# Performance work log

Measured on AMD Instinct MI355X. Metric: run time of the kernel, lower is better.

The kernel has to match this reference:

```python
import jax, jax.numpy as jnp
import numpy as np
import math

B, T, D, H = 2, 2048, 1024, 16
DK = D // H


def _alibi_bias(n_heads, seq_len):
    # canonical ALiBi: slope_h = 2^(-8*(h+1)/n_heads), bias[h,i,j] = -slope_h * (i - j) for j<=i
    slopes = jnp.asarray([2.0 ** (-8.0 * (h + 1) / n_heads) for h in range(n_heads)], dtype=jnp.float32)
    pos = jnp.arange(seq_len, dtype=jnp.float32)
    dist = pos[None, :] - pos[:, None]              # [T, T], (j - i)
    return slopes[:, None, None] * dist[None, :, :]  # [H, T, T] (masked out above diagonal anyway)


def setup_inputs() -> dict:
    key = jax.random.key(0)
    ks = jax.random.split(key, 8)
    s = 1.0 / math.sqrt(D)
    return {
        "query": jax.random.normal(ks[0], (B, T, D), dtype=jnp.float32),
        "key": jax.random.normal(ks[1], (B, T, D), dtype=jnp.float32),
        "value": jax.random.normal(ks[2], (B, T, D), dtype=jnp.float32),
        "alibi_bias": _alibi_bias(H, T),
        "Wq": jax.random.normal(ks[3], (D, D), dtype=jnp.float32) * s,
        "Wk": jax.random.normal(ks[4], (D, D), dtype=jnp.float32) * s,
        "Wv": jax.random.normal(ks[5], (D, D), dtype=jnp.float32) * s,
        "Wo": jax.random.normal(ks[6], (D, D), dtype=jnp.float32) * s,
        "bo": jnp.zeros((D,), dtype=jnp.float32),
    }


def reference(query, key, value, alibi_bias, Wq, Wk, Wv, Wo, bo):
    b, tq, d = query.shape
    tk = key.shape[1]
    # projections (torch Linear: x @ W.T)
    Q = (query @ Wq.T).reshape(b, tq, H, DK).transpose(0, 2, 1, 3)  # [B,H,Tq,dk]
    K = (key @ Wk.T).reshape(b, tk, H, DK).transpose(0, 2, 1, 3)
    V = (value @ Wv.T).reshape(b, tk, H, DK).transpose(0, 2, 1, 3)
    scores = jnp.einsum("bhqd,bhkd->bhqk", Q, K) / math.sqrt(DK)   # [B,H,Tq,Tk]
    scores = scores + alibi_bias[None]
    causal = jnp.triu(jnp.ones((tq, tk), dtype=bool), 1)
    scores = jnp.where(causal, jnp.float32(-jnp.inf), scores)
    attn = jax.nn.softmax(scores, axis=-1)
    out = jnp.einsum("bhqk,bhkd->bhqd", attn, V)                   # [B,H,Tq,dk]
    out = out.transpose(0, 2, 1, 3).reshape(b, tq, d)
    return out @ Wo.T + bo
```

## Files before the change

### kernel.cpp

```cpp
#include <hip/hip_runtime.h>
#include <hip/hip_bf16.h>


#define B_  2
#define T_  2048
#define D_  1024
#define H_  16
#define DK_ 64
#define M_  (B_ * T_)

typedef unsigned short u16;
typedef __attribute__((ext_vector_type(8))) short bf16x8;
typedef __attribute__((ext_vector_type(4))) float f32x4;

#define GL16(g, l) __builtin_amdgcn_global_load_lds( \
    (const __attribute__((address_space(1))) unsigned int*)(const void*)(g), \
    (__attribute__((address_space(3))) unsigned int*)(void*)(l), 16, 0, 0)

__device__ __constant__ float d_slopes[16] = {
    0.70710678118654752440f, 0.5f, 0.35355339059327376220f, 0.25f,
    0.17677669529663688110f, 0.125f, 0.088388347648318440550f, 0.0625f,
    0.044194173824159220275f, 0.03125f, 0.022097086912079610137f, 0.015625f,
    0.011048543456039805068f, 0.0078125f, 0.0055242717280199025342f, 0.00390625f};

__device__ __forceinline__ u16 f2bf_bits(float v) {
    union { __hip_bfloat16 h; u16 u; } cv;
    cv.h = __float2bfloat16(v);
    return cv.u;
}

__global__ __launch_bounds__(256) void cvt_all(
    const float* __restrict__ q, const float* __restrict__ k, const float* __restrict__ v,
    const float* __restrict__ wq, const float* __restrict__ wk,
    const float* __restrict__ wv, const float* __restrict__ wo,
    u16* __restrict__ xq, u16* __restrict__ xk, u16* __restrict__ xv,
    u16* __restrict__ uq, u16* __restrict__ uk, u16* __restrict__ uv, u16* __restrict__ uo) {
    const int b = blockIdx.x;
    const float* s; u16* d; int rel;
    if      (b < 2048) { s = q;  d = xq; rel = b; }
    else if (b < 4096) { s = k;  d = xk; rel = b - 2048; }
    else if (b < 6144) { s = v;  d = xv; rel = b - 4096; }
    else if (b < 6656) { s = wq; d = uq; rel = b - 6144; }
    else if (b < 7168) { s = wk; d = uk; rel = b - 6656; }
    else if (b < 7680) { s = wv; d = uv; rel = b - 7168; }
    else               { s = wo; d = uo; rel = b - 7680; }
    const size_t base = (size_t)rel * 2048 + threadIdx.x * 8;
    float4 f0 = *(const float4*)(s + base);
    float4 f1 = *(const float4*)(s + base + 4);
    alignas(16) u16 o[8];
    o[0] = f2bf_bits(f0.x); o[1] = f2bf_bits(f0.y); o[2] = f2bf_bits(f0.z); o[3] = f2bf_bits(f0.w);
    o[4] = f2bf_bits(f1.x); o[5] = f2bf_bits(f1.y); o[6] = f2bf_bits(f1.z); o[7] = f2bf_bits(f1.w);
    *(uint4*)(d + base) = *(const uint4*)o;
}

__global__ __launch_bounds__(256) void gemm_qkv(
    const u16* __restrict__ xq, const u16* __restrict__ xk, const u16* __restrict__ xv,
    const u16* __restrict__ wq, const u16* __restrict__ wk, const u16* __restrict__ wv,
    u16* __restrict__ oq, u16* __restrict__ ok, u16* __restrict__ ov) {
    __shared__ u16 smem[8704];
    u16* As = smem;
    u16* Bs = smem + 4096;

    const int z = blockIdx.z;
    const u16* X = (z == 0) ? xq : (z == 1) ? xk : xv;
    const u16* W = (z == 0) ? wq : (z == 1) ? wk : wv;

    const int tid = threadIdx.x, lane = tid & 63, w = tid >> 6;
    const int l15 = lane & 15, quad = lane >> 4;
    const int wm = w >> 1, wn = w & 1;
    const int m0 = blockIdx.y * 128, n0 = blockIdx.x * 128;
    const int srow = lane >> 2;
    const int skseg = (lane & 3) * 8;

    f32x4 acc[4][4];
#pragma unroll
    for (int mi = 0; mi < 4; ++mi)
#pragma unroll
        for (int ni = 0; ni < 4; ++ni) acc[mi][ni] = f32x4{0.f, 0.f, 0.f, 0.f};

    const u16* ga = X + (size_t)(m0 + w * 32 + srow) * D_ + skseg;
    const u16* gb = W + (size_t)(n0 + w * 32 + srow) * D_ + skseg;
    u16* lA = As + (w * 32) * 32;
    u16* lB = Bs + (w * 32) * 32;

    for (int k0 = 0; k0 < D_; k0 += 32) {
        GL16(ga + k0,             lA);
        GL16(ga + k0 + 16 * D_,   lA + 16 * 32);
        GL16(gb + k0,             lB);
        GL16(gb + k0 + 16 * D_,   lB + 16 * 32);
        __syncthreads();
        bf16x8 af[4], bfr[4];
#pragma unroll
        for (int mi = 0; mi < 4; ++mi)
            af[mi] = *(const bf16x8*)&As[(wm * 64 + mi * 16 + l15) * 32 + quad * 8];
#pragma unroll
        for (int ni = 0; ni < 4; ++ni)
            bfr[ni] = *(const bf16x8*)&Bs[(wn * 64 + ni * 16 + l15) * 32 + quad * 8];
#pragma unroll
        for (int mi = 0; mi < 4; ++mi)
#pragma unroll
            for (int ni = 0; ni < 4; ++ni)
                acc[mi][ni] = __builtin_amdgcn_mfma_f32_16x16x32_bf16(af[mi], bfr[ni], acc[mi][ni], 0, 0, 0);
        __syncthreads();
    }

    if (z < 2) {
        u16* out = (z == 0) ? oq : ok;
#pragma unroll
        for (int mi = 0; mi < 4; ++mi) {
            const int gmb = m0 + wm * 64 + mi * 16 + quad * 4;
#pragma unroll
            for (int ni = 0; ni < 4; ++ni) {
                const int gn = n0 + wn * 64 + ni * 16 + l15;
                const int h = gn >> 6, dk = gn & 63;
#pragma unroll
                for (int r = 0; r < 4; ++r) {
                    const int gm = gmb + r;
                    const int b = gm >> 11, t = gm & (T_ - 1);
                    out[(((size_t)b * H_ + h) * T_ + t) * DK_ + dk] = f2bf_bits(acc[mi][ni][r]);
                }
            }
        }
    } else {
        u16* Cs = smem;
#pragma unroll
        for (int h2 = 0; h2 < 2; ++h2) {
            __syncthreads();
            if (wn == h2) {
#pragma unroll
                for (int mi = 0; mi < 4; ++mi) {
#pragma unroll
                    for (int ni = 0; ni < 4; ++ni) {
                        const int nloc = ni * 16 + l15;
                        const int mloc = wm * 64 + mi * 16 + quad * 4;
                        alignas(8) u16 pk[4];
#pragma unroll
                        for (int r = 0; r < 4; ++r) pk[r] = f2bf_bits(acc[mi][ni][r]);
                        *(uint2*)&Cs[nloc * 136 + mloc] = *(const uint2*)pk;
                    }
                }
            }
            __syncthreads();
            const int nr = tid >> 2;
            const int mseg = (tid & 3) * 32;
            const int gn = n0 + h2 * 64 + nr;
            const int h = gn >> 6, dk = gn & 63;
            const int b = m0 >> 11;
            const int tl = (m0 & (T_ - 1)) + mseg;
            uint4 v0 = *(const uint4*)&Cs[nr * 136 + mseg];
            uint4 v1 = *(const uint4*)&Cs[nr * 136 + mseg + 8];
            uint4 v2 = *(const uint4*)&Cs[nr * 136 + mseg + 16];
            uint4 v3 = *(const uint4*)&Cs[nr * 136 + mseg + 24];
            u16* op = ov + ((size_t)(b * H_ + h) * DK_ + dk) * T_ + tl;
            *(uint4*)op = v0; *(uint4*)(op + 8) = v1;
            *(uint4*)(op + 16) = v2; *(uint4*)(op + 24) = v3;
        }
    }
}

__global__ __launch_bounds__(256) void gemm_out(const u16* __restrict__ X,
                                                const u16* __restrict__ W,
                                                const float* __restrict__ bias,
                                                float* __restrict__ out) {
    __shared__ u16 As[128 * 32];
    __shared__ u16 Bs[64 * 32];

    const int tid = threadIdx.x, lane = tid & 63, w = tid >> 6;
    const int l15 = lane & 15, quad = lane >> 4;
    const int wm = w >> 1, wn = w & 1;
    const int m0 = blockIdx.y * 128, n0 = blockIdx.x * 64;
    const int srow = lane >> 2;
    const int skseg = (lane & 3) * 8;

    f32x4 acc[4][2];
#pragma unroll
    for (int mi = 0; mi < 4; ++mi)
#pragma unroll
        for (int ni = 0; ni < 2; ++ni) acc[mi][ni] = f32x4{0.f, 0.f, 0.f, 0.f};

    const u16* ga = X + (size_t)(m0 + w * 32 + srow) * D_ + skseg;
    const u16* gb = W + (size_t)(n0 + w * 16 + srow) * D_ + skseg;
    u16* lA = As + (w * 32) * 32;
    u16* lB = Bs + (w * 16) * 32;

    for (int k0 = 0; k0 < D_; k0 += 32) {
        GL16(ga + k0,           lA);
        GL16(ga + k0 + 16 * D_, lA + 16 * 32);
        GL16(gb + k0,           lB);
        __syncthreads();
        bf16x8 af[4], bfr[2];
#pragma unroll
        for (int mi = 0; mi < 4; ++mi)
            af[mi] = *(const bf16x8*)&As[(wm * 64 + mi * 16 + l15) * 32 + quad * 8];
#pragma unroll
        for (int ni = 0; ni < 2; ++ni)
            bfr[ni] = *(const bf16x8*)&Bs[(wn * 32 + ni * 16 + l15) * 32 + quad * 8];
#pragma unroll
        for (int mi = 0; mi < 4; ++mi)
#pragma unroll
            for (int ni = 0; ni < 2; ++ni)
                acc[mi][ni] = __builtin_amdgcn_mfma_f32_16x16x32_bf16(af[mi], bfr[ni], acc[mi][ni], 0, 0, 0);
        __syncthreads();
    }

#pragma unroll
    for (int mi = 0; mi < 4; ++mi) {
        const int gmb = m0 + wm * 64 + mi * 16 + quad * 4;
#pragma unroll
        for (int ni = 0; ni < 2; ++ni) {
            const int gn = n0 + wn * 32 + ni * 16 + l15;
            const float bv = bias[gn];
#pragma unroll
            for (int r = 0; r < 4; ++r)
                out[(size_t)(gmb + r) * D_ + gn] = acc[mi][ni][r] + bv;
        }
    }
}

__global__ __launch_bounds__(256, 2) void flash_attn(const u16* __restrict__ Q,
                                                     const u16* __restrict__ K,
                                                     const u16* __restrict__ VT,
                                                     u16* __restrict__ ctx) {
    const int bh = blockIdx.x;
    const int b  = bh >> 4;
    const int h  = bh & 15;
    const int tid = threadIdx.x;
    const int wave = tid >> 6;
    const int lane = tid & 63;
    const int l15 = lane & 15;
    const int quad = lane >> 4;
    const int qt = gridDim.y - 1 - blockIdx.y;
    const int qb = qt * 64 + wave * 16;
    const float slope = d_slopes[h];

    __shared__ u16 Kl[128 * 72];
    __shared__ u16 Vl[64 * 136];
    __shared__ u16 Pl[4][16 * 136];
    u16* pl = Pl[wave];

    const size_t baseQK = (size_t)bh * T_ * DK_;
    const u16* Kg = K + baseQK;
    const u16* Vg = VT + (size_t)bh * DK_ * T_;

    const u16* qptr = Q + baseQK + (size_t)(qb + l15) * DK_ + quad * 8;
    bf16x8 aq0 = *(const bf16x8*)qptr;
    bf16x8 aq1 = *(const bf16x8*)(qptr + 32);

    const int krow = tid >> 3;
    const int kseg = (tid & 7) * 8;
    const int vrow = tid >> 4;
    const int vseg = (tid & 15) * 8;

    f32x4 o[4], osum;
#pragma unroll
    for (int t = 0; t < 4; ++t) o[t] = f32x4{0.f, 0.f, 0.f, 0.f};
    osum = f32x4{0.f, 0.f, 0.f, 0.f};

    const f32x4 zero = {0.f, 0.f, 0.f, 0.f};
    bf16x8 ones;
#pragma unroll
    for (int i = 0; i < 8; ++i) ones[i] = (short)0x3F80;

    const int kend = qt * 64 + 64;
    for (int kb = 0; kb < kend; kb += 128) {
        uint4 kreg[4], vreg[4];
#pragma unroll
        for (int p = 0; p < 4; ++p)
            kreg[p] = *(const uint4*)(Kg + (size_t)(kb + p * 32 + krow) * DK_ + kseg);
#pragma unroll
        for (int p = 0; p < 4; ++p)
            vreg[p] = *(const uint4*)(Vg + (size_t)(p * 16 + vrow) * T_ + kb + vseg);
        __syncthreads();
#pragma unroll
        for (int p = 0; p < 4; ++p)
            *(uint4*)&Kl[(p * 32 + krow) * 72 + kseg] = kreg[p];
#pragma unroll
        for (int p = 0; p < 4; ++p)
            *(uint4*)&Vl[(p * 16 + vrow) * 136 + vseg] = vreg[p];
        __syncthreads();

        if (kb < qb + 16) {
            f32x4 s[8];
#pragma unroll
            for (int t = 0; t < 8; ++t) {
                bf16x8 bk0 = *(const bf16x8*)&Kl[(t * 16 + l15) * 72 + quad * 8];
                bf16x8 bk1 = *(const bf16x8*)&Kl[(t * 16 + l15) * 72 + 32 + quad * 8];
                s[t] = __builtin_amdgcn_mfma_f32_16x16x32_bf16(aq0, bk0, zero, 0, 0, 0);
                s[t] = __builtin_amdgcn_mfma_f32_16x16x32_bf16(aq1, bk1, s[t], 0, 0, 0);
            }
#pragma unroll
            for (int t = 0; t < 8; ++t) {
#pragma unroll
                for (int r = 0; r < 4; ++r) {
                    const int row = qb + quad * 4 + r;
                    const int c = kb + t * 16 + l15;
                    const float v = s[t][r] * 0.125f + slope * (float)(c - row);
                    const float p = (c <= row) ? __expf(v) : 0.f;
                    pl[(quad * 4 + r) * 136 + t * 16 + l15] = f2bf_bits(p);
                }
            }
            bf16x8 ap[4];
#pragma unroll
            for (int g = 0; g < 4; ++g)
                ap[g] = *(const bf16x8*)&pl[l15 * 136 + g * 32 + quad * 8];
#pragma unroll
            for (int t = 0; t < 4; ++t)
#pragma unroll
                for (int g = 0; g < 4; ++g) {
                    bf16x8 bv = *(const bf16x8*)&Vl[(t * 16 + l15) * 136 + g * 32 + quad * 8];
                    o[t] = __builtin_amdgcn_mfma_f32_16x16x32_bf16(ap[g], bv, o[t], 0, 0, 0);
                }
#pragma unroll
            for (int g = 0; g < 4; ++g)
                osum = __builtin_amdgcn_mfma_f32_16x16x32_bf16(ap[g], ones, osum, 0, 0, 0);
        }
    }

#pragma unroll
    for (int r = 0; r < 4; ++r) {
        const float inv = 1.0f / osum[r];
        const int row = qb + quad * 4 + r;
        u16* cp = ctx + ((size_t)b * T_ + row) * D_ + h * DK_ + l15;
#pragma unroll
        for (int t = 0; t < 4; ++t) cp[t * 16] = f2bf_bits(o[t][r] * inv);
    }
}

extern "C" void kernel_launch(void* const* d_in, const int* in_sizes, int n_in,
                              void* d_out, int out_size, void* d_ws, size_t ws_size,
                              hipStream_t stream) {
    const float* query = (const float*)d_in[0];
    const float* key   = (const float*)d_in[1];
    const float* value = (const float*)d_in[2];
    const float* Wq    = (const float*)d_in[4];
    const float* Wk    = (const float*)d_in[5];
    const float* Wv    = (const float*)d_in[6];
    const float* Wo    = (const float*)d_in[7];
    const float* bo    = (const float*)d_in[8];
    float* out = (float*)d_out;

    const size_t elems  = (size_t)B_ * H_ * T_ * DK_;
    const size_t welems = (size_t)D_ * D_;
    u16* Qb   = (u16*)d_ws;
    u16* Kb   = Qb + elems;
    u16* VTb  = Kb + elems;
    u16* ctxb = VTb + elems;
    u16* Xq   = ctxb + elems;
    u16* Xk   = Xq + elems;
    u16* Xv   = Xk + elems;
    u16* Uq   = Xv + elems;
    u16* Uk   = Uq + welems;
    u16* Uv   = Uk + welems;
    u16* Uo   = Uv + welems;

    dim3 blk(256);
    cvt_all<<<8192, blk, 0, stream>>>(query, key, value, Wq, Wk, Wv, Wo,
                                      Xq, Xk, Xv, Uq, Uk, Uv, Uo);
    gemm_qkv<<<dim3(D_ / 128, M_ / 128, 3), blk, 0, stream>>>(Xq, Xk, Xv, Uq, Uk, Uv, Qb, Kb, VTb);
    flash_attn<<<dim3(B_ * H_, T_ / 64), blk, 0, stream>>>(Qb, Kb, VTb, ctxb);
    gemm_out<<<dim3(D_ / 64, M_ / 128), blk, 0, stream>>>(ctxb, Uo, bo, out);
}
```

Measured before the change: 506.5 us.

## Skip masked key tiles and fold softmax scale into Wq with exp2

Folds the 1/sqrt(dk)·log2(e) factor into Wq during bf16 conversion and pre-multiplies the ALiBi slopes by log2(e), so the softmax uses exp2f with precomputed per-lane bias terms. The score MFMA operands are swapped so each lane writes a packed 4-element row of P. Per-wave loops now stop at the last causal 16-column tile, skipping QK, PV and row-sum MFMAs on fully masked tiles, and masking is applied only on the diagonal tile. The launch-bounds occupancy hint is dropped, and the data-dependent breaks in unrolled loops may cost extra branching.

```diff
diff --git a/kernel.cpp b/kernel.cpp
--- a/kernel.cpp
+++ b/kernel.cpp
@@ -10,6 +10,7 @@
 #define M_  (B_ * T_)
 
 typedef unsigned short u16;
+typedef unsigned int u32;
 typedef __attribute__((ext_vector_type(8))) short bf16x8;
 typedef __attribute__((ext_vector_type(4))) float f32x4;
 
@@ -17,11 +18,25 @@
     (const __attribute__((address_space(1))) unsigned int*)(const void*)(g), \
     (__attribute__((address_space(3))) unsigned int*)(void*)(l), 16, 0, 0)
 
-__device__ __constant__ float d_slopes[16] = {
-    0.70710678118654752440f, 0.5f, 0.35355339059327376220f, 0.25f,
-    0.17677669529663688110f, 0.125f, 0.088388347648318440550f, 0.0625f,
-    0.044194173824159220275f, 0.03125f, 0.022097086912079610137f, 0.015625f,
-    0.011048543456039805068f, 0.0078125f, 0.0055242717280199025342f, 0.00390625f};
+__device__ __constant__ float d_slopes2[16] = {
+    (float)(0.70710678118654752440 * 1.4426950408889634074),
+    (float)(0.5 * 1.4426950408889634074),
+    (float)(0.35355339059327376220 * 1.4426950408889634074),
+    (float)(0.25 * 1.4426950408889634074),
+    (float)(0.17677669529663688110 * 1.4426950408889634074),
+    (float)(0.125 * 1.4426950408889634074),
+    (float)(0.088388347648318440550 * 1.4426950408889634074),
+    (float)(0.0625 * 1.4426950408889634074),
+    (float)(0.044194173824159220275 * 1.4426950408889634074),
+    (float)(0.03125 * 1.4426950408889634074),
+    (float)(0.022097086912079610137 * 1.4426950408889634074),
+    (float)(0.015625 * 1.4426950408889634074),
+    (float)(0.011048543456039805068 * 1.4426950408889634074),
+    (float)(0.0078125 * 1.4426950408889634074),
+    (float)(0.0055242717280199025342 * 1.4426950408889634074),
+    (float)(0.00390625 * 1.4426950408889634074)};
+
+#define QSCALE 0.18033688013889634f
 
 __device__ __forceinline__ u16 f2bf_bits(float v) {
     union { __hip_bfloat16 h; u16 u; } cv;
@@ -36,11 +51,11 @@
     u16* __restrict__ xq, u16* __restrict__ xk, u16* __restrict__ xv,
     u16* __restrict__ uq, u16* __restrict__ uk, u16* __restrict__ uv, u16* __restrict__ uo) {
     const int b = blockIdx.x;
-    const float* s; u16* d; int rel;
+    const float* s; u16* d; int rel; float scl = 1.0f;
     if      (b < 2048) { s = q;  d = xq; rel = b; }
     else if (b < 4096) { s = k;  d = xk; rel = b - 2048; }
     else if (b < 6144) { s = v;  d = xv; rel = b - 4096; }
-    else if (b < 6656) { s = wq; d = uq; rel = b - 6144; }
+    else if (b < 6656) { s = wq; d = uq; rel = b - 6144; scl = QSCALE; }
     else if (b < 7168) { s = wk; d = uk; rel = b - 6656; }
     else if (b < 7680) { s = wv; d = uv; rel = b - 7168; }
     else               { s = wo; d = uo; rel = b - 7680; }
@@ -48,8 +63,10 @@
     float4 f0 = *(const float4*)(s + base);
     float4 f1 = *(const float4*)(s + base + 4);
     alignas(16) u16 o[8];
-    o[0] = f2bf_bits(f0.x); o[1] = f2bf_bits(f0.y); o[2] = f2bf_bits(f0.z); o[3] = f2bf_bits(f0.w);
-    o[4] = f2bf_bits(f1.x); o[5] = f2bf_bits(f1.y); o[6] = f2bf_bits(f1.z); o[7] = f2bf_bits(f1.w);
+    o[0] = f2bf_bits(f0.x * scl); o[1] = f2bf_bits(f0.y * scl);
+    o[2] = f2bf_bits(f0.z * scl); o[3] = f2bf_bits(f0.w * scl);
+    o[4] = f2bf_bits(f1.x * scl); o[5] = f2bf_bits(f1.y * scl);
+    o[6] = f2bf_bits(f1.z * scl); o[7] = f2bf_bits(f1.w * scl);
     *(uint4*)(d + base) = *(const uint4*)o;
 }
 
@@ -217,10 +234,10 @@
     }
 }
 
-__global__ __launch_bounds__(256, 2) void flash_attn(const u16* __restrict__ Q,
-                                                     const u16* __restrict__ K,
-                                                     const u16* __restrict__ VT,
-                                                     u16* __restrict__ ctx) {
+__global__ __launch_bounds__(256) void flash_attn(const u16* __restrict__ Q,
+                                                  const u16* __restrict__ K,
+                                                  const u16* __restrict__ VT,
+                                                  u16* __restrict__ ctx) {
     const int bh = blockIdx.x;
     const int b  = bh >> 4;
     const int h  = bh & 15;
@@ -231,7 +248,8 @@
     const int quad = lane >> 4;
     const int qt = gridDim.y - 1 - blockIdx.y;
     const int qb = qt * 64 + wave * 16;
-    const float slope = d_slopes[h];
+    const float sl2 = d_slopes2[h];
+    const float sl2_16 = sl2 * 16.0f;
 
     __shared__ u16 Kl[128 * 72];
     __shared__ u16 Vl[64 * 136];
@@ -246,6 +264,14 @@
     bf16x8 aq0 = *(const bf16x8*)qptr;
     bf16x8 aq1 = *(const bf16x8*)(qptr + 32);
 
+    float aqr[4]; bool mskr[4];
+#pragma unroll
+    for (int r = 0; r < 4; ++r) {
+        const int dqr = quad * 4 + r - l15;
+        aqr[r]  = sl2 * (float)dqr;
+        mskr[r] = dqr <= 0;
+    }
+
     const int krow = tid >> 3;
     const int kseg = (tid & 7) * 8;
     const int vrow = tid >> 4;
@@ -279,40 +305,65 @@
             *(uint4*)&Vl[(p * 16 + vrow) * 136 + vseg] = vreg[p];
         __syncthreads();
 
-        if (kb < qb + 16) {
+        const int dd = qb - kb;
+        if (dd >= 0) {
+            const int nt = (dd >> 4) + 1;
+            const int gmax = (nt + 1) >> 1;
+
             f32x4 s[8];
 #pragma unroll
             for (int t = 0; t < 8; ++t) {
+                if (t >= nt) break;
                 bf16x8 bk0 = *(const bf16x8*)&Kl[(t * 16 + l15) * 72 + quad * 8];
                 bf16x8 bk1 = *(const bf16x8*)&Kl[(t * 16 + l15) * 72 + 32 + quad * 8];
-                s[t] = __builtin_amdgcn_mfma_f32_16x16x32_bf16(aq0, bk0, zero, 0, 0, 0);
-                s[t] = __builtin_amdgcn_mfma_f32_16x16x32_bf16(aq1, bk1, s[t], 0, 0, 0);
-            }
+                s[t] = __builtin_amdgcn_mfma_f32_16x16x32_bf16(bk0, aq0, zero, 0, 0, 0);
+                s[t] = __builtin_amdgcn_mfma_f32_16x16x32_bf16(bk1, aq1, s[t], 0, 0, 0);
+            }
+
+            const float cb = sl2 * (float)(-dd);
 #pragma unroll
             for (int t = 0; t < 8; ++t) {
-#pragma unroll
-                for (int r = 0; r < 4; ++r) {
-                    const int row = qb + quad * 4 + r;
-                    const int c = kb + t * 16 + l15;
-                    const float v = s[t][r] * 0.125f + slope * (float)(c - row);
-                    const float p = (c <= row) ? __expf(v) : 0.f;
-                    pl[(quad * 4 + r) * 136 + t * 16 + l15] = f2bf_bits(p);
+                if (t >= nt) break;
+                float p[4];
+                if (t < nt - 1) {
+                    const float bt = cb + sl2_16 * (float)t;
+#pragma unroll
+                    for (int r = 0; r < 4; ++r)
+                        p[r] = exp2f(s[t][r] + (aqr[r] + bt));
+                } else {
+#pragma unroll
+                    for (int r = 0; r < 4; ++r) {
+                        const float e = exp2f(s[t][r] + aqr[r]);
+                        p[r] = mskr[r] ? e : 0.f;
+                    }
                 }
-            }
+                const u32 lo = (u32)f2bf_bits(p[0]) | ((u32)f2bf_bits(p[1]) << 16);
+                const u32 hi = (u32)f2bf_bits(p[2]) | ((u32)f2bf_bits(p[3]) << 16);
+                *(uint2*)&pl[l15 * 136 + t * 16 + quad * 4] = make_uint2(lo, hi);
+            }
+            if (nt < 8 && (nt & 1))
+                *(uint2*)&pl[l15 * 136 + nt * 16 + quad * 4] = make_uint2(0u, 0u);
+
             bf16x8 ap[4];
 #pragma unroll
-            for (int g = 0; g < 4; ++g)
+            for (int g = 0; g < 4; ++g) {
+                if (g >= gmax) break;
                 ap[g] = *(const bf16x8*)&pl[l15 * 136 + g * 32 + quad * 8];
-#pragma unroll
-            for (int t = 0; t < 4; ++t)
+            }
+#pragma unroll
+            for (int dt = 0; dt < 4; ++dt) {
 #pragma unroll
                 for (int g = 0; g < 4; ++g) {
-                    bf16x8 bv = *(const bf16x8*)&Vl[(t * 16 + l15) * 136 + g * 32 + quad * 8];
-                    o[t] = __builtin_amdgcn_mfma_f32_16x16x32_bf16(ap[g], bv, o[t], 0, 0, 0);
+                    if (g >= gmax) break;
+                    bf16x8 bv = *(const bf16x8*)&Vl[(dt * 16 + l15) * 136 + g * 32 + quad * 8];
+                    o[dt] = __builtin_amdgcn_mfma_f32_16x16x32_bf16(ap[g], bv, o[dt], 0, 0, 0);
                 }
-#pragma unroll
-            for (int g = 0; g < 4; ++g)
+            }
+#pragma unroll
+            for (int g = 0; g < 4; ++g) {
+                if (g >= gmax) break;
                 osum = __builtin_amdgcn_mfma_f32_16x16x32_bf16(ap[g], ones, osum, 0, 0, 0);
+            }
         }
     }
 
```

After: 514.1 us. Within noise of the previous version (+1.5%).
